# Kernel optimization log

Hardware: AMD Instinct MI355X
Metric: run time of the kernel (lower is better)

## Reference

```python
import jax, jax.numpy as jnp
import numpy as np

B, SIG, L, LAT, ENC_H, DEC_H, RHS_H, T = 256, 64, 1024, 256, 256, 512, 512, 200


def setup_inputs() -> dict:
    key = jax.random.key(0)
    ks = jax.random.split(key, 32)
    p = lambda k, s: jax.random.normal(k, s, dtype=jnp.float32) * 0.05
    inp = {
        'y': jax.random.normal(ks[0], (B, SIG, L), dtype=jnp.float32),
        't': jnp.arange(T, dtype=jnp.float32) * 0.01,
        # encoder: conv3 (OIH) + bias, res conv1 + bias, 3 layers
        'ew0': p(ks[1], (ENC_H, SIG, 3)), 'eb0': p(ks[2], (ENC_H,)),
        'rw0': p(ks[3], (ENC_H, SIG, 1)), 'rb0': p(ks[4], (ENC_H,)),
        'ew1': p(ks[5], (ENC_H, ENC_H, 3)), 'eb1': p(ks[6], (ENC_H,)),
        'rw1': p(ks[7], (ENC_H, ENC_H, 1)), 'rb1': p(ks[8], (ENC_H,)),
        'ew2': p(ks[9], (LAT, ENC_H, 3)), 'eb2': p(ks[10], (LAT,)),
        'rw2': p(ks[11], (LAT, ENC_H, 1)), 'rb2': p(ks[12], (LAT,)),
        # rhs MLP: LAT -> RHS_H -> RHS_H -> LAT
        'fw0': p(ks[13], (RHS_H, LAT)), 'fb0': p(ks[14], (RHS_H,)),
        'fw1': p(ks[15], (RHS_H, RHS_H)), 'fb1': p(ks[16], (RHS_H,)),
        'fw2': p(ks[17], (LAT, RHS_H)), 'fb2': p(ks[18], (LAT,)),
        # decoder MLP: LAT -> DEC_H -> DEC_H -> SIG
        'dw0': p(ks[19], (DEC_H, LAT)), 'db0': p(ks[20], (DEC_H,)),
        'dw1': p(ks[21], (DEC_H, DEC_H)), 'db1': p(ks[22], (DEC_H,)),
        'dw2': p(ks[23], (SIG, DEC_H)), 'db2': p(ks[24], (SIG,)),
    }
    return inp


def _conv1d(x, w, b, pad):
    out = jax.lax.conv_general_dilated(x, w, window_strides=(1,), padding=[(pad, pad)],
                                       dimension_numbers=('NCH', 'OIH', 'NCH'))
    return out + b[None, :, None]


def _forward(y, t, ew0, eb0, rw0, rb0, ew1, eb1, rw1, rb1, ew2, eb2, rw2, rb2,
             fw0, fb0, fw1, fb1, fw2, fb2, dw0, db0, dw1, db1, dw2, db2):
    # --- encoder: residual conv blocks; tanh on all but last ---
    x = y
    for (cw, cb, rw, rb, act) in [(ew0, eb0, rw0, rb0, True),
                                  (ew1, eb1, rw1, rb1, True),
                                  (ew2, eb2, rw2, rb2, False)]:
        out = _conv1d(x, cw, cb, 1)
        x = _conv1d(x, rw, rb, 0) + out
        if act:
            x = jnp.tanh(x)
    z0 = x[:, :, 0]  # [B, LAT]

    # --- RHS MLP (autonomous) ---
    def rhs(z):
        h = jnp.tanh(z @ fw0.T + fb0)
        h = jnp.tanh(h @ fw1.T + fb1)
        return h @ fw2.T + fb2

    # --- fixed-grid RK4 odeint over t ---
    def step(z, ts):
        t0, t1 = ts
        h = t1 - t0
        k1 = rhs(z)
        k2 = rhs(z + 0.5 * h * k1)
        k3 = rhs(z + 0.5 * h * k2)
        k4 = rhs(z + h * k3)
        z = z + (h / 6.0) * (k1 + 2.0 * k2 + 2.0 * k3 + k4)
        return z, z

    _, zs = jax.lax.scan(step, z0, (t[:-1], t[1:]))
    pred_z = jnp.concatenate([z0[None], zs], axis=0)  # [T, B, LAT]

    # --- decoder MLP ---
    h = jnp.tanh(pred_z @ dw0.T + db0)
    h = jnp.tanh(h @ dw1.T + db1)
    pred_y = h @ dw2.T + db2  # [T, B, SIG]
    return jnp.transpose(pred_y, (1, 2, 0))  # [B, SIG, T]


def reference(y, t, ew0, eb0, rw0, rb0, ew1, eb1, rw1, rb1, ew2, eb2, rw2, rb2,
              fw0, fb0, fw1, fb1, fw2, fb2, dw0, db0, dw1, db1, dw2, db2):
    return _forward(y, t, ew0, eb0, rw0, rb0, ew1, eb1, rw1, rb1, ew2, eb2, rw2, rb2,
                    fw0, fb0, fw1, fb1, fw2, fb2, dw0, db0, dw1, db1, dw2, db2)
```

## Files before the change

### kernel.cpp

```cpp
#include <hip/hip_runtime.h>
#include <hip/hip_bf16.h>

typedef unsigned short u16;

#define B_      256
#define SIG_    64
#define L_      1024
#define LAT_    256
#define RHSH_   512
#define T_      200

__device__ __forceinline__ bool probe_bf16(const void* tptr) {
    return ((const unsigned*)tptr)[0] != 0u;
}
__device__ __forceinline__ float ld_flex(const void* p, size_t i, bool bf) {
    return bf ? __bfloat162float(((const __hip_bfloat16*)p)[i]) : ((const float*)p)[i];
}
__device__ __forceinline__ u16 f2bf(float f) {
    unsigned x = __float_as_uint(f);
    unsigned r = x + 0x7FFFu + ((x >> 16) & 1u);
    return (u16)(r >> 16);
}
__device__ __forceinline__ float bf2f(u16 v) {
    return __uint_as_float((unsigned)v << 16);
}

static constexpr size_t Z0F  = 0;
static constexpr size_t EW0T = Z0F  + 65536;
static constexpr size_t RW0T = EW0T + 49152;
static constexpr size_t EW1T = RW0T + 16384;
static constexpr size_t RW1T = EW1T + 196608;
static constexpr size_t EW2T = RW1T + 65536;
static constexpr size_t RW2T = EW2T + 196608;
static constexpr size_t CB0  = RW2T + 65536;
static constexpr size_t CB1  = CB0 + 256;
static constexpr size_t CB2  = CB1 + 256;
static constexpr size_t TFO  = CB2 + 256;
static constexpr size_t FB0  = TFO + 256;
static constexpr size_t FB1  = FB0 + 512;
static constexpr size_t FB2  = FB1 + 512;
static constexpr size_t DB0  = FB2 + 256;
static constexpr size_t DB1  = DB0 + 512;
static constexpr size_t DB2  = DB1 + 512;
static constexpr size_t SALT = DB2 + 64;
static constexpr size_t FP32_END = SALT + 16;

static constexpr size_t FW0NS = 0;
static constexpr size_t FW1NS = FW0NS + 131072;
static constexpr size_t FW2NS = FW1NS + 262144;
static constexpr size_t DW0B  = FW2NS + 131072;
static constexpr size_t DW1B  = DW0B + 131072;
static constexpr size_t DW2B  = DW1B + 262144;
static constexpr size_t ZS    = DW2B + 32768;
static constexpr size_t US_END = ZS + 13107200;

static constexpr size_t EXCH_U64_PER_PAIR = 2048;
static constexpr size_t EXCH_OFF  = FP32_END * 4 + US_END * 2;
static constexpr size_t EXCH_BYTES = 128 * EXCH_U64_PER_PAIR * 8;
static constexpr size_t NEED_BYTES = EXCH_OFF + EXCH_BYTES;

__global__ void k_transpose(const void* __restrict__ in, float* __restrict__ out,
                            int N, int K, const void* __restrict__ tp) {
    bool bf = probe_bf16(tp);
    int idx = blockIdx.x * 256 + threadIdx.x;
    if (idx < N * K) {
        int k = idx / N;
        int n = idx - k * N;
        out[idx] = ld_flex(in, (size_t)n * K + k, bf);
    }
}

__global__ void k_prep_wns(const void* __restrict__ in, u16* __restrict__ out,
                           int N, int K, const void* __restrict__ tp) {
    bool bf = probe_bf16(tp);
    int idx = blockIdx.x * 256 + threadIdx.x;
    if (idx >= N * K) return;
    int NH = N >> 1;
    int c = idx % NH;
    int k = (idx / NH) % K;
    int h = idx / (NH * K);
    float v = ld_flex(in, (size_t)(h * NH + c) * K + k, bf);
    out[idx] = f2bf(v);
}

__global__ void k_prep_wtb(const void* __restrict__ in, u16* __restrict__ out,
                           int N, int K, const void* __restrict__ tp) {
    bool bf = probe_bf16(tp);
    int idx = blockIdx.x * 256 + threadIdx.x;
    if (idx >= N * K) return;
    int n = idx % N;
    int k = idx / N;
    out[idx] = f2bf(ld_flex(in, (size_t)n * K + k, bf));
}

__global__ void k_cvt(const void* __restrict__ in, float* __restrict__ out, int n,
                      const void* __restrict__ tp) {
    bool bf = probe_bf16(tp);
    int i = blockIdx.x * 256 + threadIdx.x;
    if (i < n) out[i] = ld_flex(in, i, bf);
}

__global__ void k_cvt_add(const void* __restrict__ a, const void* __restrict__ b,
                          float* __restrict__ out, int n, const void* __restrict__ tp) {
    bool bf = probe_bf16(tp);
    int i = blockIdx.x * 256 + threadIdx.x;
    if (i < n) out[i] = ld_flex(a, i, bf) + ld_flex(b, i, bf);
}

__global__ void k_fill(float* __restrict__ out, int n, float v) {
    int i = blockIdx.x * 256 + threadIdx.x;
    if (i < n) out[i] = v;
}

__global__ void k_bump(unsigned* p) {
    if (threadIdx.x == 0) p[0] = p[0] + 1u;
}

__global__ __launch_bounds__(256) void k_encoder(
    const void* __restrict__ y, const void* __restrict__ tp,
    const float* __restrict__ ew0T, const float* __restrict__ rw0T, const float* __restrict__ cb0,
    const float* __restrict__ ew1T, const float* __restrict__ rw1T, const float* __restrict__ cb1,
    const float* __restrict__ ew2T, const float* __restrict__ rw2T, const float* __restrict__ cb2,
    float* __restrict__ z0f) {
    bool bf = probe_bf16(tp);
    int b = blockIdx.x;
    int o = threadIdx.x;
    __shared__ float ys[64][4];
    __shared__ float x1[3][256];
    __shared__ float x2[2][256];

    {
        int i = o >> 2, l = o & 3;
        ys[i][l] = ld_flex(y, (size_t)b * SIG_ * L_ + (size_t)i * L_ + l, bf);
    }
    __syncthreads();

    {
        float a0 = 0.f, a1 = 0.f, a2 = 0.f;
        for (int i = 0; i < 64; i++) {
            float w0 = ew0T[(i * 3 + 0) * 256 + o];
            float w1 = ew0T[(i * 3 + 1) * 256 + o];
            float w2 = ew0T[(i * 3 + 2) * 256 + o];
            float rw = rw0T[i * 256 + o];
            float v0 = ys[i][0], v1 = ys[i][1], v2 = ys[i][2], v3 = ys[i][3];
            a0 += w1 * v0 + w2 * v1 + rw * v0;
            a1 += w0 * v0 + w1 * v1 + w2 * v2 + rw * v1;
            a2 += w0 * v1 + w1 * v2 + w2 * v3 + rw * v2;
        }
        float cb = cb0[o];
        x1[0][o] = tanhf(a0 + cb);
        x1[1][o] = tanhf(a1 + cb);
        x1[2][o] = tanhf(a2 + cb);
    }
    __syncthreads();

    {
        float a0 = 0.f, a1 = 0.f;
        for (int i = 0; i < 256; i++) {
            float w0 = ew1T[(i * 3 + 0) * 256 + o];
            float w1 = ew1T[(i * 3 + 1) * 256 + o];
            float w2 = ew1T[(i * 3 + 2) * 256 + o];
            float rw = rw1T[i * 256 + o];
            float v0 = x1[0][i], v1 = x1[1][i], v2 = x1[2][i];
            a0 += w1 * v0 + w2 * v1 + rw * v0;
            a1 += w0 * v0 + w1 * v1 + w2 * v2 + rw * v1;
        }
        float cb = cb1[o];
        x2[0][o] = tanhf(a0 + cb);
        x2[1][o] = tanhf(a1 + cb);
    }
    __syncthreads();

    {
        float a0 = 0.f;
        for (int i = 0; i < 256; i++) {
            float w1 = ew2T[(i * 3 + 1) * 256 + o];
            float w2 = ew2T[(i * 3 + 2) * 256 + o];
            float rw = rw2T[i * 256 + o];
            a0 += w1 * x2[0][i] + w2 * x2[1][i] + rw * x2[0][i];
        }
        z0f[(size_t)b * 256 + o] = a0 + cb2[o];
    }
}

#define RM_NONE 0
#define RM_PLAIN 1
#define RM_S1 2
#define RM_S2 3
#define RM_S34 4
#define TL_PLAIN 0
#define TL_RK 1
#define TL_K4 2

template <int KIN, int NOUT, bool ACT, int RM, int TL>
__device__ __forceinline__ void layer_ns(
    float* xs,
    const u16* __restrict__ wb,
    const float* __restrict__ bias,
    float* xo,
    float* scratch,
    unsigned long long* __restrict__ sendBuf,
    const unsigned long long* __restrict__ recvBuf,
    unsigned sendTag, unsigned recvTag, int nHalf, int tid,
    float* zbL, float* acL, float* ztL,
    float rcAC, float rcZT,
    bool tInit, float tcAC, float tcZT,
    u16* zsOut) {
    constexpr int NH  = NOUT / 2;
    constexpr int CQ  = NH / 4;
    constexpr int NPH = 512 / CQ;
    constexpr int KH  = KIN / 2;
    constexpr int KC2 = KH / NPH;
    constexpr int WK  = KH / 8;
    const int cq = tid & (CQ - 1);
    const int ph = tid / CQ;
    const int locB = nHalf * KH;
    const int remB = KH - locB;
    const u16* wl = wb + ((size_t)(locB + ph * KC2)) * NH + 4 * cq;
    const u16* wr = wb + ((size_t)(remB + ph * KC2)) * NH + 4 * cq;
    const float* xl0 = xs + locB + ph * KC2;
    const float* xl1 = xs + KIN + locB + ph * KC2;
    float4 a0 = {0.f, 0.f, 0.f, 0.f}, a1 = {0.f, 0.f, 0.f, 0.f};
#pragma unroll 4
    for (int k = 0; k < KC2; k++) {
        uint2 w = *(const uint2*)(wl + (size_t)k * NH);
        float w0 = __uint_as_float(w.x << 16);
        float w1 = __uint_as_float(w.x & 0xFFFF0000u);
        float w2 = __uint_as_float(w.y << 16);
        float w3 = __uint_as_float(w.y & 0xFFFF0000u);
        float v0 = xl0[k], v1 = xl1[k];
        a0.x += v0 * w0; a0.y += v0 * w1; a0.z += v0 * w2; a0.w += v0 * w3;
        a1.x += v1 * w0; a1.y += v1 * w1; a1.z += v1 * w2; a1.w += v1 * w3;
    }
    if constexpr (RM != RM_NONE) {
        const int lane = tid & 63;
        const int wave = tid >> 6;
        if (lane < 2 * WK) {
            const int r = lane / WK;
            const int kRel = wave * WK + (lane % WK);
            unsigned long long p;
            for (;;) {
                p = __hip_atomic_load(&recvBuf[r * KH + kRel],
                                      __ATOMIC_RELAXED, __HIP_MEMORY_SCOPE_AGENT);
                if ((unsigned)(p >> 32) == recvTag) break;
                __builtin_amdgcn_s_sleep(2);
            }
            float kv = __uint_as_float((unsigned)p);
            const int xi = r * KIN + remB + kRel;
            if constexpr (RM == RM_PLAIN) {
                xs[xi] = kv;
            } else if constexpr (RM == RM_S1) {
                xs[xi] = acL[xi] + rcAC * kv;
            } else if constexpr (RM == RM_S2) {
                float zv = zbL[xi];
                acL[xi] = zv + rcAC * kv;
                xs[xi] = zv + rcZT * kv;
            } else {
                float zv = zbL[xi];
                acL[xi] += rcAC * kv;
                xs[xi] = zv + rcZT * kv;
            }
        }
    }
    const float* xr0 = xs + remB + ph * KC2;
    const float* xr1 = xs + KIN + remB + ph * KC2;
#pragma unroll 4
    for (int k = 0; k < KC2; k++) {
        uint2 w = *(const uint2*)(wr + (size_t)k * NH);
        float w0 = __uint_as_float(w.x << 16);
        float w1 = __uint_as_float(w.x & 0xFFFF0000u);
        float w2 = __uint_as_float(w.y << 16);
        float w3 = __uint_as_float(w.y & 0xFFFF0000u);
        float v0 = xr0[k], v1 = xr1[k];
        a0.x += v0 * w0; a0.y += v0 * w1; a0.z += v0 * w2; a0.w += v0 * w3;
        a1.x += v1 * w0; a1.y += v1 * w1; a1.z += v1 * w2; a1.w += v1 * w3;
    }
    *(float4*)(scratch + (size_t)(ph * 2 + 0) * NH + 4 * cq) = a0;
    *(float4*)(scratch + (size_t)(ph * 2 + 1) * NH + 4 * cq) = a1;
    __syncthreads();
    if (tid < 2 * NH) {
        const int r = tid / NH, c = tid % NH;
        float s = 0.f;
#pragma unroll
        for (int p = 0; p < NPH; p++) s += scratch[(size_t)(p * 2 + r) * NH + c];
        s += bias[c];
        if constexpr (TL == TL_PLAIN) {
            if (ACT) s = tanhf(s);
            xo[r * NOUT + nHalf * NH + c] = s;
        }
        {
            unsigned long long packed =
                ((unsigned long long)sendTag << 32) | (unsigned long long)__float_as_uint(s);
            __hip_atomic_store(&sendBuf[r * NH + c], packed,
                               __ATOMIC_RELAXED, __HIP_MEMORY_SCOPE_AGENT);
        }
        if constexpr (TL == TL_RK) {
            const int zi = r * 256 + nHalf * NH + c;
            float zv = zbL[zi];
            acL[zi] = (tInit ? zv : acL[zi]) + tcAC * s;
            ztL[zi] = zv + tcZT * s;
        } else if constexpr (TL == TL_K4) {
            const int zi = r * 256 + nHalf * NH + c;
            float zn = acL[zi] + tcAC * s;
            zbL[zi] = zn;
            zsOut[zi] = f2bf(zn);
        }
    }
    __syncthreads();
}

__global__ __launch_bounds__(512) void k_ode_ns(
    const u16* __restrict__ fw0ns, const float* __restrict__ fb0,
    const u16* __restrict__ fw1ns, const float* __restrict__ fb1,
    const u16* __restrict__ fw2ns, const float* __restrict__ fb2,
    const float* __restrict__ tf, const float* __restrict__ z0f,
    const unsigned* __restrict__ saltp,
    u16* __restrict__ zs, unsigned long long* __restrict__ ex) {
    __shared__ __align__(16) float zb[512];
    __shared__ __align__(16) float zt[512];
    __shared__ __align__(16) float ac[512];
    __shared__ __align__(16) float h1[1024];
    __shared__ __align__(16) float h2[1024];
    __shared__ __align__(16) float scratch[4096];

    const int tid = threadIdx.x;
    const int pairId = blockIdx.x & 127;
    const int nHalf  = blockIdx.x >> 7;
    const int row0 = pairId * 2;
    unsigned long long* exBase = ex + (size_t)pairId * EXCH_U64_PER_PAIR;

    const unsigned salt = __hip_atomic_load(saltp, __ATOMIC_RELAXED, __HIP_MEMORY_SCOPE_AGENT);
    unsigned tag = salt << 13;

#define SB(t) (exBase + ((size_t)(nHalf * 2 + ((t) & 1)) * 512))
#define RB(t) ((const unsigned long long*)(exBase + ((size_t)((1 - nHalf) * 2 + ((t) & 1)) * 512)))

    const u16* fw0w = fw0ns + (size_t)nHalf * 256 * 256;
    const u16* fw1w = fw1ns + (size_t)nHalf * 512 * 256;
    const u16* fw2w = fw2ns + (size_t)nHalf * 512 * 128;
    const float* fb0o = fb0 + nHalf * 256;
    const float* fb1o = fb1 + nHalf * 256;
    const float* fb2o = fb2 + nHalf * 128;

    zb[tid] = z0f[(size_t)(row0 + (tid >> 8)) * 256 + (tid & 255)];
    __syncthreads();

    if (tid < 256) {
        int r = tid >> 7, c = tid & 127;
        zs[(size_t)(row0 + r) * 256 + nHalf * 128 + c] = f2bf(zb[r * 256 + nHalf * 128 + c]);
    }

    float h6prev = 0.f;
    unsigned tcPrev = 0;

    for (int t = 0; t < T_ - 1; t++) {
        float hstep = tf[t + 1] - tf[t];
        float hh = 0.5f * hstep;
        float h3 = hstep * (1.0f / 3.0f);
        float h6 = hstep * (1.0f / 6.0f);

        unsigned ta, tb, tc;
        ta = ++tag; tb = ++tag; tc = ++tag;
        if (t == 0)
            layer_ns<256, 512, true, RM_NONE, TL_PLAIN>(zb, fw0w, fb0o, h1, scratch,
                SB(ta), nullptr, ta, 0u, nHalf, tid, zb, ac, zt, 0.f, 0.f, false, 0.f, 0.f, nullptr);
        else
            layer_ns<256, 512, true, RM_S1, TL_PLAIN>(zb, fw0w, fb0o, h1, scratch,
                SB(ta), RB(tcPrev), ta, tcPrev, nHalf, tid, zb, ac, zt, h6prev, 0.f, false, 0.f, 0.f, nullptr);
        layer_ns<512, 512, true, RM_PLAIN, TL_PLAIN>(h1, fw1w, fb1o, h2, scratch,
            SB(tb), RB(ta), tb, ta, nHalf, tid, zb, ac, zt, 0.f, 0.f, false, 0.f, 0.f, nullptr);
        layer_ns<512, 256, false, RM_PLAIN, TL_RK>(h2, fw2w, fb2o, nullptr, scratch,
            SB(tc), RB(tb), tc, tb, nHalf, tid, zb, ac, zt, 0.f, 0.f, true, h6, hh, nullptr);
        tcPrev = tc;

        ta = ++tag; tb = ++tag; tc = ++tag;
        layer_ns<256, 512, true, RM_S2, TL_PLAIN>(zt, fw0w, fb0o, h1, scratch,
            SB(ta), RB(tcPrev), ta, tcPrev, nHalf, tid, zb, ac, zt, h6, hh, false, 0.f, 0.f, nullptr);
        layer_ns<512, 512, true, RM_PLAIN, TL_PLAIN>(h1, fw1w, fb1o, h2, scratch,
            SB(tb), RB(ta), tb, ta, nHalf, tid, zb, ac, zt, 0.f, 0.f, false, 0.f, 0.f, nullptr);
        layer_ns<512, 256, false, RM_PLAIN, TL_RK>(h2, fw2w, fb2o, nullptr, scratch,
            SB(tc), RB(tb), tc, tb, nHalf, tid, zb, ac, zt, 0.f, 0.f, false, h3, hh, nullptr);
        tcPrev = tc;

        ta = ++tag; tb = ++tag; tc = ++tag;
        layer_ns<256, 512, true, RM_S34, TL_PLAIN>(zt, fw0w, fb0o, h1, scratch,
            SB(ta), RB(tcPrev), ta, tcPrev, nHalf, tid, zb, ac, zt, h3, hh, false, 0.f, 0.f, nullptr);
        layer_ns<512, 512, true, RM_PLAIN, TL_PLAIN>(h1, fw1w, fb1o, h2, scratch,
            SB(tb), RB(ta), tb, ta, nHalf, tid, zb, ac, zt, 0.f, 0.f, false, 0.f, 0.f, nullptr);
        layer_ns<512, 256, false, RM_PLAIN, TL_RK>(h2, fw2w, fb2o, nullptr, scratch,
            SB(tc), RB(tb), tc, tb, nHalf, tid, zb, ac, zt, 0.f, 0.f, false, h3, hstep, nullptr);
        tcPrev = tc;

        ta = ++tag; tb = ++tag; tc = ++tag;
        layer_ns<256, 512, true, RM_S34, TL_PLAIN>(zt, fw0w, fb0o, h1, scratch,
            SB(ta), RB(tcPrev), ta, tcPrev, nHalf, tid, zb, ac, zt, h3, hstep, false, 0.f, 0.f, nullptr);
        layer_ns<512, 512, true, RM_PLAIN, TL_PLAIN>(h1, fw1w, fb1o, h2, scratch,
            SB(tb), RB(ta), tb, ta, nHalf, tid, zb, ac, zt, 0.f, 0.f, false, 0.f, 0.f, nullptr);
        layer_ns<512, 256, false, RM_PLAIN, TL_K4>(h2, fw2w, fb2o, nullptr, scratch,
            SB(tc), RB(tb), tc, tb, nHalf, tid, zb, ac, zt, 0.f, 0.f, false, h6, 0.f,
            zs + (size_t)(t + 1) * 65536 + (size_t)row0 * 256);
        tcPrev = tc;
        h6prev = h6;
    }
#undef SB
#undef RB
}

template <int K>
__device__ __forceinline__ void dec_layer512(
    const float* xin, const u16* __restrict__ wt, const float* __restrict__ bias,
    float* xout, int tid) {
    const int q = tid & 127;
    const int g = tid >> 7;
    const u16* wp = wt + 4 * q;
    const float* xr = xin + (size_t)g * 5 * K;
    float4 a[5];
#pragma unroll
    for (int r = 0; r < 5; r++) a[r] = {0.f, 0.f, 0.f, 0.f};
#pragma unroll 4
    for (int k = 0; k < K; k++) {
        uint2 w = *(const uint2*)(wp + (size_t)k * 512);
        float w0 = __uint_as_float(w.x << 16);
        float w1 = __uint_as_float(w.x & 0xFFFF0000u);
        float w2 = __uint_as_float(w.y << 16);
        float w3 = __uint_as_float(w.y & 0xFFFF0000u);
#pragma unroll
        for (int r = 0; r < 5; r++) {
            float v = xr[r * K + k];
            a[r].x += v * w0; a[r].y += v * w1; a[r].z += v * w2; a[r].w += v * w3;
        }
    }
    float b0 = bias[4 * q + 0], b1 = bias[4 * q + 1], b2 = bias[4 * q + 2], b3 = bias[4 * q + 3];
#pragma unroll
    for (int r = 0; r < 5; r++) {
        float4 o;
        o.x = tanhf(a[r].x + b0);
        o.y = tanhf(a[r].y + b1);
        o.z = tanhf(a[r].z + b2);
        o.w = tanhf(a[r].w + b3);
        *(float4*)(xout + (size_t)(g * 5 + r) * 512 + 4 * q) = o;
    }
}

__global__ __launch_bounds__(512) void k_decode(
    const u16* __restrict__ zs,
    const u16* __restrict__ dw0b, const float* __restrict__ db0,
    const u16* __restrict__ dw1b, const float* __restrict__ db1,
    const u16* __restrict__ dw2b, const float* __restrict__ db2,
    float* __restrict__ out) {
    __shared__ __align__(16) float xb[20 * 256];
    __shared__ __align__(16) float hh1[20 * 512];
    __shared__ __align__(16) float hh2[20 * 512];
    const int tid = threadIdx.x;
    const int b  = blockIdx.x & 255;
    const int t0 = (blockIdx.x >> 8) * 20;

    for (int i = tid; i < 20 * 256; i += 512) {
        int r = i >> 8, k = i & 255;
        xb[i] = bf2f(zs[(size_t)(t0 + r) * 65536 + (size_t)b * 256 + k]);
    }
    __syncthreads();

    dec_layer512<256>(xb, dw0b, db0, hh1, tid);
    __syncthreads();
    dec_layer512<512>(hh1, dw1b, db1, hh2, tid);
    __syncthreads();

    if (tid < 320) {
        const int q = tid & 15;
        const int r = tid >> 4;
        const u16* wp = dw2b + 4 * q;
        const float* xr = hh2 + (size_t)r * 512;
        float4 a = {0.f, 0.f, 0.f, 0.f};
#pragma unroll 4
        for (int k = 0; k < 512; k++) {
            uint2 w = *(const uint2*)(wp + (size_t)k * 64);
            float w0 = __uint_as_float(w.x << 16);
            float w1 = __uint_as_float(w.x & 0xFFFF0000u);
            float w2 = __uint_as_float(w.y << 16);
            float w3 = __uint_as_float(w.y & 0xFFFF0000u);
            float v = xr[k];
            a.x += v * w0; a.y += v * w1; a.z += v * w2; a.w += v * w3;
        }
        const int tt = t0 + r;
        out[((size_t)b * 64 + 4 * q + 0) * 200 + tt] = a.x + db2[4 * q + 0];
        out[((size_t)b * 64 + 4 * q + 1) * 200 + tt] = a.y + db2[4 * q + 1];
        out[((size_t)b * 64 + 4 * q + 2) * 200 + tt] = a.z + db2[4 * q + 2];
        out[((size_t)b * 64 + 4 * q + 3) * 200 + tt] = a.w + db2[4 * q + 3];
    }
}

#define GRID256(n) ((((n) + 255) / 256))

static const int DICT_SIZES[26] = {
    16777216, 200, 49152, 256, 16384, 256, 196608, 256, 65536, 256,
    196608, 256, 65536, 256, 131072, 512, 262144, 512, 131072, 256,
    131072, 512, 262144, 512, 32768, 64};
static const int ALPHA_SIZES[26] = {
    512, 512, 64, 131072, 262144, 32768, 256, 256, 256, 49152,
    196608, 196608, 512, 512, 256, 131072, 262144, 131072, 256, 256,
    256, 16384, 65536, 65536, 200, 16777216};
static const int ALPHA_MAP[26] = {
    25, 24, 9, 6, 21, 18, 10, 7, 22, 19, 11, 8, 23, 20, 15, 12, 16, 13, 17, 14,
    3, 0, 4, 1, 5, 2};

extern "C" void kernel_launch(void* const* d_in, const int* in_sizes, int n_in,
                              void* d_out, int out_size, void* d_ws, size_t ws_size,
                              hipStream_t stream) {
    float* out = (float*)d_out;

    bool dict_ok = (n_in == 26), alpha_ok = (n_in == 26);
    for (int i = 0; i < 26 && i < n_in; i++) {
        if (in_sizes[i] != DICT_SIZES[i]) dict_ok = false;
        if (in_sizes[i] != ALPHA_SIZES[i]) alpha_ok = false;
    }
    const void* in[26];
    if (dict_ok) {
        for (int s = 0; s < 26; s++) in[s] = d_in[s];
    } else if (alpha_ok) {
        for (int s = 0; s < 26; s++) in[s] = d_in[ALPHA_MAP[s]];
    } else {
        k_fill<<<GRID256(out_size), 256, 0, stream>>>(out, out_size, 1000.0f);
        return;
    }
    if (ws_size < NEED_BYTES) {
        k_fill<<<GRID256(out_size), 256, 0, stream>>>(out, out_size, 500.0f);
        return;
    }

    const void* y   = in[0];
    const void* t   = in[1];
    const void* ew0 = in[2];
    const void* eb0 = in[3];
    const void* rw0 = in[4];
    const void* rb0 = in[5];
    const void* ew1 = in[6];
    const void* eb1 = in[7];
    const void* rw1 = in[8];
    const void* rb1 = in[9];
    const void* ew2 = in[10];
    const void* eb2 = in[11];
    const void* rw2 = in[12];
    const void* rb2 = in[13];
    const void* fw0 = in[14];
    const void* fb0 = in[15];
    const void* fw1 = in[16];
    const void* fb1 = in[17];
    const void* fw2 = in[18];
    const void* fb2 = in[19];
    const void* dw0 = in[20];
    const void* db0 = in[21];
    const void* dw1 = in[22];
    const void* db1 = in[23];
    const void* dw2 = in[24];
    const void* db2 = in[25];

    float* ws = (float*)d_ws;
    u16* wns = (u16*)(ws + FP32_END);
    unsigned long long* ex = (unsigned long long*)((char*)d_ws + EXCH_OFF);

    k_bump<<<1, 1, 0, stream>>>((unsigned*)(ws + SALT));

    k_transpose<<<GRID256(256 * 192), 256, 0, stream>>>(ew0, ws + EW0T, 256, 192, t);
    k_transpose<<<GRID256(256 * 64),  256, 0, stream>>>(rw0, ws + RW0T, 256, 64, t);
    k_transpose<<<GRID256(256 * 768), 256, 0, stream>>>(ew1, ws + EW1T, 256, 768, t);
    k_transpose<<<GRID256(256 * 256), 256, 0, stream>>>(rw1, ws + RW1T, 256, 256, t);
    k_transpose<<<GRID256(256 * 768), 256, 0, stream>>>(ew2, ws + EW2T, 256, 768, t);
    k_transpose<<<GRID256(256 * 256), 256, 0, stream>>>(rw2, ws + RW2T, 256, 256, t);

    k_prep_wns<<<GRID256(512 * 256), 256, 0, stream>>>(fw0, wns + FW0NS, 512, 256, t);
    k_prep_wns<<<GRID256(512 * 512), 256, 0, stream>>>(fw1, wns + FW1NS, 512, 512, t);
    k_prep_wns<<<GRID256(256 * 512), 256, 0, stream>>>(fw2, wns + FW2NS, 256, 512, t);
    k_prep_wtb<<<GRID256(512 * 256), 256, 0, stream>>>(dw0, wns + DW0B, 512, 256, t);
    k_prep_wtb<<<GRID256(512 * 512), 256, 0, stream>>>(dw1, wns + DW1B, 512, 512, t);
    k_prep_wtb<<<GRID256(64 * 512),  256, 0, stream>>>(dw2, wns + DW2B, 64, 512, t);

    k_cvt<<<GRID256(512), 256, 0, stream>>>(fb0, ws + FB0, 512, t);
    k_cvt<<<GRID256(512), 256, 0, stream>>>(fb1, ws + FB1, 512, t);
    k_cvt<<<GRID256(256), 256, 0, stream>>>(fb2, ws + FB2, 256, t);
    k_cvt<<<GRID256(512), 256, 0, stream>>>(db0, ws + DB0, 512, t);
    k_cvt<<<GRID256(512), 256, 0, stream>>>(db1, ws + DB1, 512, t);
    k_cvt<<<GRID256(64),  256, 0, stream>>>(db2, ws + DB2, 64, t);
    k_cvt<<<GRID256(200), 256, 0, stream>>>(t,   ws + TFO, 200, t);
    k_cvt_add<<<GRID256(256), 256, 0, stream>>>(eb0, rb0, ws + CB0, 256, t);
    k_cvt_add<<<GRID256(256), 256, 0, stream>>>(eb1, rb1, ws + CB1, 256, t);
    k_cvt_add<<<GRID256(256), 256, 0, stream>>>(eb2, rb2, ws + CB2, 256, t);

    k_encoder<<<B_, 256, 0, stream>>>(y, t,
        ws + EW0T, ws + RW0T, ws + CB0,
        ws + EW1T, ws + RW1T, ws + CB1,
        ws + EW2T, ws + RW2T, ws + CB2,
        ws + Z0F);

    k_ode_ns<<<256, 512, 0, stream>>>(
        wns + FW0NS, ws + FB0, wns + FW1NS, ws + FB1, wns + FW2NS, ws + FB2,
        ws + TFO, ws + Z0F, (const unsigned*)(ws + SALT),
        wns + ZS, ex);

    k_decode<<<2560, 512, 0, stream>>>(
        wns + ZS, wns + DW0B, ws + DB0, wns + DW1B, ws + DB1, wns + DW2B, ws + DB2, out);
}
```

Baseline: 9.128 ms.

## Replace paired-block ODE exchange with single-row fp16 dot2 kernel and LDS weight cache

Removes the cross-block exchange, in which two blocks each computed half the outputs for two rows and synchronised through global-memory atomics with spin-waits. Now one block per batch row runs all RK4 stages alone. Weights are packed as fp16 k-pairs so the kernel can use the fdot2 instruction, activations are packed to fp16 in LDS, and part of fw1 is cached in LDS. tanhf is replaced by an exp-based fast tanh in the ODE and decoder. This removes the inter-block synchronisation latency, but each block now streams the full weight matrices, and fp16 weights and activations plus the approximate tanh reduce precision.

```diff
diff --git a/kernel.cpp b/kernel.cpp
--- a/kernel.cpp
+++ b/kernel.cpp
@@ -23,6 +23,32 @@
 }
 __device__ __forceinline__ float bf2f(u16 v) {
     return __uint_as_float((unsigned)v << 16);
+}
+
+typedef _Float16 half2_t __attribute__((ext_vector_type(2)));
+
+#if defined(__has_builtin)
+#if __has_builtin(__builtin_amdgcn_fdot2)
+#define HAVE_FDOT2 1
+#endif
+#endif
+
+__device__ __forceinline__ float fdot2(unsigned w, unsigned x, float c) {
+#ifdef HAVE_FDOT2
+    return __builtin_amdgcn_fdot2(__builtin_bit_cast(half2_t, w),
+                                  __builtin_bit_cast(half2_t, x), c, false);
+#else
+    half2_t a = __builtin_bit_cast(half2_t, w);
+    half2_t b = __builtin_bit_cast(half2_t, x);
+    return c + (float)a.x * (float)b.x + (float)a.y * (float)b.y;
+#endif
+}
+__device__ __forceinline__ unsigned pk16(float a, float b) {
+    return __builtin_bit_cast(unsigned, __builtin_amdgcn_cvt_pkrtz(a, b));
+}
+__device__ __forceinline__ float fast_tanh(float x) {
+    float e = __expf(2.0f * x);
+    return 1.0f - 2.0f / (e + 1.0f);
 }
 
 static constexpr size_t Z0F  = 0;
@@ -42,22 +68,18 @@
 static constexpr size_t DB0  = FB2 + 256;
 static constexpr size_t DB1  = DB0 + 512;
 static constexpr size_t DB2  = DB1 + 512;
-static constexpr size_t SALT = DB2 + 64;
-static constexpr size_t FP32_END = SALT + 16;
-
-static constexpr size_t FW0NS = 0;
-static constexpr size_t FW1NS = FW0NS + 131072;
-static constexpr size_t FW2NS = FW1NS + 262144;
-static constexpr size_t DW0B  = FW2NS + 131072;
+static constexpr size_t FP32_END = DB2 + 64 + 16;
+
+static constexpr size_t FW0KP = 0;
+static constexpr size_t FW1KP = FW0KP + 131072;
+static constexpr size_t FW2KP = FW1KP + 262144;
+static constexpr size_t DW0B  = FW2KP + 131072;
 static constexpr size_t DW1B  = DW0B + 131072;
 static constexpr size_t DW2B  = DW1B + 262144;
 static constexpr size_t ZS    = DW2B + 32768;
 static constexpr size_t US_END = ZS + 13107200;
 
-static constexpr size_t EXCH_U64_PER_PAIR = 2048;
-static constexpr size_t EXCH_OFF  = FP32_END * 4 + US_END * 2;
-static constexpr size_t EXCH_BYTES = 128 * EXCH_U64_PER_PAIR * 8;
-static constexpr size_t NEED_BYTES = EXCH_OFF + EXCH_BYTES;
+static constexpr size_t NEED_BYTES = FP32_END * 4 + US_END * 2;
 
 __global__ void k_transpose(const void* __restrict__ in, float* __restrict__ out,
                             int N, int K, const void* __restrict__ tp) {
@@ -70,17 +92,18 @@
     }
 }
 
-__global__ void k_prep_wns(const void* __restrict__ in, u16* __restrict__ out,
+__global__ void k_prep_wkp(const void* __restrict__ in, u16* __restrict__ out,
                            int N, int K, const void* __restrict__ tp) {
     bool bf = probe_bf16(tp);
     int idx = blockIdx.x * 256 + threadIdx.x;
     if (idx >= N * K) return;
-    int NH = N >> 1;
-    int c = idx % NH;
-    int k = (idx / NH) % K;
-    int h = idx / (NH * K);
-    float v = ld_flex(in, (size_t)(h * NH + c) * K + k, bf);
-    out[idx] = f2bf(v);
+    int kp = idx & 1;
+    int n  = (idx >> 1) % N;
+    int k2 = (idx >> 1) / N;
+    int k  = 2 * k2 + kp;
+    float v = ld_flex(in, (size_t)n * K + k, bf);
+    _Float16 hv = (_Float16)v;
+    out[idx] = *(u16*)&hv;
 }
 
 __global__ void k_prep_wtb(const void* __restrict__ in, u16* __restrict__ out,
@@ -110,10 +133,6 @@
 __global__ void k_fill(float* __restrict__ out, int n, float v) {
     int i = blockIdx.x * 256 + threadIdx.x;
     if (i < n) out[i] = v;
-}
-
-__global__ void k_bump(unsigned* p) {
-    if (threadIdx.x == 0) p[0] = p[0] + 1u;
 }
 
 __global__ __launch_bounds__(256) void k_encoder(
@@ -183,227 +202,157 @@
     }
 }
 
-#define RM_NONE 0
-#define RM_PLAIN 1
-#define RM_S1 2
-#define RM_S2 3
-#define RM_S34 4
 #define TL_PLAIN 0
 #define TL_RK 1
 #define TL_K4 2
 
-template <int KIN, int NOUT, bool ACT, int RM, int TL>
-__device__ __forceinline__ void layer_ns(
-    float* xs,
-    const u16* __restrict__ wb,
+#define DOT4(W4, XA) \
+    a.x = fdot2((W4).x, (XA), a.x); a.y = fdot2((W4).y, (XA), a.y); \
+    a.z = fdot2((W4).z, (XA), a.z); a.w = fdot2((W4).w, (XA), a.w);
+
+template <int KIN, int NOUT, bool ACT, bool ZIN, int TL, bool WC>
+__device__ __forceinline__ void layer_f(
+    const float* zin,
+    const unsigned* xpin,
+    const unsigned* __restrict__ w,
     const float* __restrict__ bias,
-    float* xo,
+    unsigned* xpo,
     float* scratch,
-    unsigned long long* __restrict__ sendBuf,
-    const unsigned long long* __restrict__ recvBuf,
-    unsigned sendTag, unsigned recvTag, int nHalf, int tid,
+    const unsigned* w1c,
+    int tid,
     float* zbL, float* acL, float* ztL,
-    float rcAC, float rcZT,
-    bool tInit, float tcAC, float tcZT,
-    u16* zsOut) {
-    constexpr int NH  = NOUT / 2;
-    constexpr int CQ  = NH / 4;
+    bool tInit, float tcAC, float tcZT, u16* zsOut) {
+    constexpr int CQ  = NOUT / 4;
     constexpr int NPH = 512 / CQ;
-    constexpr int KH  = KIN / 2;
-    constexpr int KC2 = KH / NPH;
-    constexpr int WK  = KH / 8;
+    constexpr int KC  = KIN / NPH;
+    constexpr int K2C = KC / 2;
     const int cq = tid & (CQ - 1);
     const int ph = tid / CQ;
-    const int locB = nHalf * KH;
-    const int remB = KH - locB;
-    const u16* wl = wb + ((size_t)(locB + ph * KC2)) * NH + 4 * cq;
-    const u16* wr = wb + ((size_t)(remB + ph * KC2)) * NH + 4 * cq;
-    const float* xl0 = xs + locB + ph * KC2;
-    const float* xl1 = xs + KIN + locB + ph * KC2;
-    float4 a0 = {0.f, 0.f, 0.f, 0.f}, a1 = {0.f, 0.f, 0.f, 0.f};
-#pragma unroll 4
-    for (int k = 0; k < KC2; k++) {
-        uint2 w = *(const uint2*)(wl + (size_t)k * NH);
-        float w0 = __uint_as_float(w.x << 16);
-        float w1 = __uint_as_float(w.x & 0xFFFF0000u);
-        float w2 = __uint_as_float(w.y << 16);
-        float w3 = __uint_as_float(w.y & 0xFFFF0000u);
-        float v0 = xl0[k], v1 = xl1[k];
-        a0.x += v0 * w0; a0.y += v0 * w1; a0.z += v0 * w2; a0.w += v0 * w3;
-        a1.x += v1 * w0; a1.y += v1 * w1; a1.z += v1 * w2; a1.w += v1 * w3;
-    }
-    if constexpr (RM != RM_NONE) {
-        const int lane = tid & 63;
-        const int wave = tid >> 6;
-        if (lane < 2 * WK) {
-            const int r = lane / WK;
-            const int kRel = wave * WK + (lane % WK);
-            unsigned long long p;
-            for (;;) {
-                p = __hip_atomic_load(&recvBuf[r * KH + kRel],
-                                      __ATOMIC_RELAXED, __HIP_MEMORY_SCOPE_AGENT);
-                if ((unsigned)(p >> 32) == recvTag) break;
-                __builtin_amdgcn_s_sleep(2);
+    const unsigned* wp = w + (size_t)(ph * K2C) * NOUT + 4 * cq;
+    float4 a = {0.f, 0.f, 0.f, 0.f};
+    if constexpr (ZIN) {
+        const float* x0 = zin + ph * KC;
+#pragma unroll 16
+        for (int j = 0; j < K2C; j++) {
+            uint4 w4 = *(const uint4*)(wp + (size_t)j * NOUT);
+            float2 p0 = *(const float2*)(x0 + 2 * j);
+            unsigned xa = pk16(p0.x, p0.y);
+            DOT4(w4, xa)
+        }
+    } else if constexpr (WC) {
+        const unsigned* q0 = xpin + ph * K2C;
+        if (ph == 0) {
+            const unsigned* wl = w1c + 4 * cq;
+#pragma unroll 16
+            for (int j = 0; j < K2C; j++) {
+                uint4 w4 = *(const uint4*)(wl + (size_t)j * NOUT);
+                unsigned xa = q0[j];
+                DOT4(w4, xa)
             }
-            float kv = __uint_as_float((unsigned)p);
-            const int xi = r * KIN + remB + kRel;
-            if constexpr (RM == RM_PLAIN) {
-                xs[xi] = kv;
-            } else if constexpr (RM == RM_S1) {
-                xs[xi] = acL[xi] + rcAC * kv;
-            } else if constexpr (RM == RM_S2) {
-                float zv = zbL[xi];
-                acL[xi] = zv + rcAC * kv;
-                xs[xi] = zv + rcZT * kv;
-            } else {
-                float zv = zbL[xi];
-                acL[xi] += rcAC * kv;
-                xs[xi] = zv + rcZT * kv;
+        } else {
+#pragma unroll 16
+            for (int j = 0; j < K2C; j++) {
+                uint4 w4 = *(const uint4*)(wp + (size_t)j * NOUT);
+                unsigned xa = q0[j];
+                DOT4(w4, xa)
             }
         }
-    }
-    const float* xr0 = xs + remB + ph * KC2;
-    const float* xr1 = xs + KIN + remB + ph * KC2;
-#pragma unroll 4
-    for (int k = 0; k < KC2; k++) {
-        uint2 w = *(const uint2*)(wr + (size_t)k * NH);
-        float w0 = __uint_as_float(w.x << 16);
-        float w1 = __uint_as_float(w.x & 0xFFFF0000u);
-        float w2 = __uint_as_float(w.y << 16);
-        float w3 = __uint_as_float(w.y & 0xFFFF0000u);
-        float v0 = xr0[k], v1 = xr1[k];
-        a0.x += v0 * w0; a0.y += v0 * w1; a0.z += v0 * w2; a0.w += v0 * w3;
-        a1.x += v1 * w0; a1.y += v1 * w1; a1.z += v1 * w2; a1.w += v1 * w3;
-    }
-    *(float4*)(scratch + (size_t)(ph * 2 + 0) * NH + 4 * cq) = a0;
-    *(float4*)(scratch + (size_t)(ph * 2 + 1) * NH + 4 * cq) = a1;
-    __syncthreads();
-    if (tid < 2 * NH) {
-        const int r = tid / NH, c = tid % NH;
+    } else {
+        const unsigned* q0 = xpin + ph * K2C;
+#pragma unroll 16
+        for (int j = 0; j < K2C; j++) {
+            uint4 w4 = *(const uint4*)(wp + (size_t)j * NOUT);
+            unsigned xa = q0[j];
+            DOT4(w4, xa)
+        }
+    }
+    *(float4*)(scratch + (size_t)ph * NOUT + 4 * cq) = a;
+    __syncthreads();
+    if (tid < NOUT) {
+        const int c = tid;
         float s = 0.f;
 #pragma unroll
-        for (int p = 0; p < NPH; p++) s += scratch[(size_t)(p * 2 + r) * NH + c];
+        for (int p = 0; p < NPH; p++) s += scratch[(size_t)p * NOUT + c];
         s += bias[c];
+        if (ACT) s = fast_tanh(s);
         if constexpr (TL == TL_PLAIN) {
-            if (ACT) s = tanhf(s);
-            xo[r * NOUT + nHalf * NH + c] = s;
-        }
-        {
-            unsigned long long packed =
-                ((unsigned long long)sendTag << 32) | (unsigned long long)__float_as_uint(s);
-            __hip_atomic_store(&sendBuf[r * NH + c], packed,
-                               __ATOMIC_RELAXED, __HIP_MEMORY_SCOPE_AGENT);
-        }
-        if constexpr (TL == TL_RK) {
-            const int zi = r * 256 + nHalf * NH + c;
-            float zv = zbL[zi];
-            acL[zi] = (tInit ? zv : acL[zi]) + tcAC * s;
-            ztL[zi] = zv + tcZT * s;
-        } else if constexpr (TL == TL_K4) {
-            const int zi = r * 256 + nHalf * NH + c;
-            float zn = acL[zi] + tcAC * s;
-            zbL[zi] = zn;
-            zsOut[zi] = f2bf(zn);
-        }
-    }
-    __syncthreads();
-}
-
-__global__ __launch_bounds__(512) void k_ode_ns(
-    const u16* __restrict__ fw0ns, const float* __restrict__ fb0,
-    const u16* __restrict__ fw1ns, const float* __restrict__ fb1,
-    const u16* __restrict__ fw2ns, const float* __restrict__ fb2,
+            float sn = __shfl_down(s, 1);
+            if ((tid & 1) == 0) xpo[c >> 1] = pk16(s, sn);
+        } else if constexpr (TL == TL_RK) {
+            float zv = zbL[c];
+            acL[c] = (tInit ? zv : acL[c]) + tcAC * s;
+            ztL[c] = zv + tcZT * s;
+        } else {
+            float zn = acL[c] + tcAC * s;
+            zbL[c] = zn;
+            zsOut[c] = f2bf(zn);
+        }
+    }
+    __syncthreads();
+}
+
+__global__ __launch_bounds__(512) void k_ode_f(
+    const u16* __restrict__ fw0, const float* __restrict__ fb0,
+    const u16* __restrict__ fw1, const float* __restrict__ fb1,
+    const u16* __restrict__ fw2, const float* __restrict__ fb2,
     const float* __restrict__ tf, const float* __restrict__ z0f,
-    const unsigned* __restrict__ saltp,
-    u16* __restrict__ zs, unsigned long long* __restrict__ ex) {
-    __shared__ __align__(16) float zb[512];
-    __shared__ __align__(16) float zt[512];
-    __shared__ __align__(16) float ac[512];
-    __shared__ __align__(16) float h1[1024];
-    __shared__ __align__(16) float h2[1024];
-    __shared__ __align__(16) float scratch[4096];
+    u16* __restrict__ zs) {
+    __shared__ __align__(16) float zb[256];
+    __shared__ __align__(16) float zt[256];
+    __shared__ __align__(16) float ac[256];
+    __shared__ __align__(16) unsigned h1p[256];
+    __shared__ __align__(16) unsigned h2p[256];
+    __shared__ __align__(16) float scratch[2048];
+    __shared__ __align__(16) unsigned w1c[32768];
 
     const int tid = threadIdx.x;
-    const int pairId = blockIdx.x & 127;
-    const int nHalf  = blockIdx.x >> 7;
-    const int row0 = pairId * 2;
-    unsigned long long* exBase = ex + (size_t)pairId * EXCH_U64_PER_PAIR;
-
-    const unsigned salt = __hip_atomic_load(saltp, __ATOMIC_RELAXED, __HIP_MEMORY_SCOPE_AGENT);
-    unsigned tag = salt << 13;
-
-#define SB(t) (exBase + ((size_t)(nHalf * 2 + ((t) & 1)) * 512))
-#define RB(t) ((const unsigned long long*)(exBase + ((size_t)((1 - nHalf) * 2 + ((t) & 1)) * 512)))
-
-    const u16* fw0w = fw0ns + (size_t)nHalf * 256 * 256;
-    const u16* fw1w = fw1ns + (size_t)nHalf * 512 * 256;
-    const u16* fw2w = fw2ns + (size_t)nHalf * 512 * 128;
-    const float* fb0o = fb0 + nHalf * 256;
-    const float* fb1o = fb1 + nHalf * 256;
-    const float* fb2o = fb2 + nHalf * 128;
-
-    zb[tid] = z0f[(size_t)(row0 + (tid >> 8)) * 256 + (tid & 255)];
-    __syncthreads();
-
-    if (tid < 256) {
-        int r = tid >> 7, c = tid & 127;
-        zs[(size_t)(row0 + r) * 256 + nHalf * 128 + c] = f2bf(zb[r * 256 + nHalf * 128 + c]);
-    }
-
-    float h6prev = 0.f;
-    unsigned tcPrev = 0;
+    const int row = blockIdx.x;
+    const unsigned* fw0u = (const unsigned*)fw0;
+    const unsigned* fw1u = (const unsigned*)fw1;
+    const unsigned* fw2u = (const unsigned*)fw2;
+
+    for (int i = tid * 4; i < 32768; i += 2048)
+        *(uint4*)&w1c[i] = *(const uint4*)&fw1u[i];
+
+    if (tid < 256) zb[tid] = z0f[(size_t)row * 256 + tid];
+    __syncthreads();
+    if (tid < 256) zs[(size_t)row * 256 + tid] = f2bf(zb[tid]);
 
     for (int t = 0; t < T_ - 1; t++) {
         float hstep = tf[t + 1] - tf[t];
         float hh = 0.5f * hstep;
         float h3 = hstep * (1.0f / 3.0f);
         float h6 = hstep * (1.0f / 6.0f);
-
-        unsigned ta, tb, tc;
-        ta = ++tag; tb = ++tag; tc = ++tag;
-        if (t == 0)
-            layer_ns<256, 512, true, RM_NONE, TL_PLAIN>(zb, fw0w, fb0o, h1, scratch,
-                SB(ta), nullptr, ta, 0u, nHalf, tid, zb, ac, zt, 0.f, 0.f, false, 0.f, 0.f, nullptr);
-        else
-            layer_ns<256, 512, true, RM_S1, TL_PLAIN>(zb, fw0w, fb0o, h1, scratch,
-                SB(ta), RB(tcPrev), ta, tcPrev, nHalf, tid, zb, ac, zt, h6prev, 0.f, false, 0.f, 0.f, nullptr);
-        layer_ns<512, 512, true, RM_PLAIN, TL_PLAIN>(h1, fw1w, fb1o, h2, scratch,
-            SB(tb), RB(ta), tb, ta, nHalf, tid, zb, ac, zt, 0.f, 0.f, false, 0.f, 0.f, nullptr);
-        layer_ns<512, 256, false, RM_PLAIN, TL_RK>(h2, fw2w, fb2o, nullptr, scratch,
-            SB(tc), RB(tb), tc, tb, nHalf, tid, zb, ac, zt, 0.f, 0.f, true, h6, hh, nullptr);
-        tcPrev = tc;
-
-        ta = ++tag; tb = ++tag; tc = ++tag;
-        layer_ns<256, 512, true, RM_S2, TL_PLAIN>(zt, fw0w, fb0o, h1, scratch,
-            SB(ta), RB(tcPrev), ta, tcPrev, nHalf, tid, zb, ac, zt, h6, hh, false, 0.f, 0.f, nullptr);
-        layer_ns<512, 512, true, RM_PLAIN, TL_PLAIN>(h1, fw1w, fb1o, h2, scratch,
-            SB(tb), RB(ta), tb, ta, nHalf, tid, zb, ac, zt, 0.f, 0.f, false, 0.f, 0.f, nullptr);
-        layer_ns<512, 256, false, RM_PLAIN, TL_RK>(h2, fw2w, fb2o, nullptr, scratch,
-            SB(tc), RB(tb), tc, tb, nHalf, tid, zb, ac, zt, 0.f, 0.f, false, h3, hh, nullptr);
-        tcPrev = tc;
-
-        ta = ++tag; tb = ++tag; tc = ++tag;
-        layer_ns<256, 512, true, RM_S34, TL_PLAIN>(zt, fw0w, fb0o, h1, scratch,
-            SB(ta), RB(tcPrev), ta, tcPrev, nHalf, tid, zb, ac, zt, h3, hh, false, 0.f, 0.f, nullptr);
-        layer_ns<512, 512, true, RM_PLAIN, TL_PLAIN>(h1, fw1w, fb1o, h2, scratch,
-            SB(tb), RB(ta), tb, ta, nHalf, tid, zb, ac, zt, 0.f, 0.f, false, 0.f, 0.f, nullptr);
-        layer_ns<512, 256, false, RM_PLAIN, TL_RK>(h2, fw2w, fb2o, nullptr, scratch,
-            SB(tc), RB(tb), tc, tb, nHalf, tid, zb, ac, zt, 0.f, 0.f, false, h3, hstep, nullptr);
-        tcPrev = tc;
-
-        ta = ++tag; tb = ++tag; tc = ++tag;
-        layer_ns<256, 512, true, RM_S34, TL_PLAIN>(zt, fw0w, fb0o, h1, scratch,
-            SB(ta), RB(tcPrev), ta, tcPrev, nHalf, tid, zb, ac, zt, h3, hstep, false, 0.f, 0.f, nullptr);
-        layer_ns<512, 512, true, RM_PLAIN, TL_PLAIN>(h1, fw1w, fb1o, h2, scratch,
-            SB(tb), RB(ta), tb, ta, nHalf, tid, zb, ac, zt, 0.f, 0.f, false, 0.f, 0.f, nullptr);
-        layer_ns<512, 256, false, RM_PLAIN, TL_K4>(h2, fw2w, fb2o, nullptr, scratch,
-            SB(tc), RB(tb), tc, tb, nHalf, tid, zb, ac, zt, 0.f, 0.f, false, h6, 0.f,
-            zs + (size_t)(t + 1) * 65536 + (size_t)row0 * 256);
-        tcPrev = tc;
-        h6prev = h6;
-    }
-#undef SB
-#undef RB
+        u16* zo = zs + (size_t)(t + 1) * 65536 + (size_t)row * 256;
+
+        layer_f<256, 512, true , true , TL_PLAIN, false>(zb, nullptr, fw0u, fb0, h1p,
+            scratch, nullptr, tid, zb, ac, zt, false, 0.f, 0.f, nullptr);
+        layer_f<512, 512, true , false, TL_PLAIN, true >(nullptr, h1p, fw1u, fb1, h2p,
+            scratch, w1c, tid, zb, ac, zt, false, 0.f, 0.f, nullptr);
+        layer_f<512, 256, false, false, TL_RK  , false>(nullptr, h2p, fw2u, fb2, nullptr,
+            scratch, nullptr, tid, zb, ac, zt, true, h6, hh, nullptr);
+
+        layer_f<256, 512, true , true , TL_PLAIN, false>(zt, nullptr, fw0u, fb0, h1p,
+            scratch, nullptr, tid, zb, ac, zt, false, 0.f, 0.f, nullptr);
+        layer_f<512, 512, true , false, TL_PLAIN, true >(nullptr, h1p, fw1u, fb1, h2p,
+            scratch, w1c, tid, zb, ac, zt, false, 0.f, 0.f, nullptr);
+        layer_f<512, 256, false, false, TL_RK  , false>(nullptr, h2p, fw2u, fb2, nullptr,
+            scratch, nullptr, tid, zb, ac, zt, false, h3, hh, nullptr);
+
+        layer_f<256, 512, true , true , TL_PLAIN, false>(zt, nullptr, fw0u, fb0, h1p,
+            scratch, nullptr, tid, zb, ac, zt, false, 0.f, 0.f, nullptr);
+        layer_f<512, 512, true , false, TL_PLAIN, true >(nullptr, h1p, fw1u, fb1, h2p,
+            scratch, w1c, tid, zb, ac, zt, false, 0.f, 0.f, nullptr);
+        layer_f<512, 256, false, false, TL_RK  , false>(nullptr, h2p, fw2u, fb2, nullptr,
+            scratch, nullptr, tid, zb, ac, zt, false, h3, hstep, nullptr);
+
+        layer_f<256, 512, true , true , TL_PLAIN, false>(zt, nullptr, fw0u, fb0, h1p,
+            scratch, nullptr, tid, zb, ac, zt, false, 0.f, 0.f, nullptr);
+        layer_f<512, 512, true , false, TL_PLAIN, true >(nullptr, h1p, fw1u, fb1, h2p,
+            scratch, w1c, tid, zb, ac, zt, false, 0.f, 0.f, nullptr);
+        layer_f<512, 256, false, false, TL_K4  , false>(nullptr, h2p, fw2u, fb2, nullptr,
+            scratch, nullptr, tid, zb, ac, zt, false, h6, 0.f, zo);
+    }
 }
 
 template <int K>
@@ -434,10 +383,10 @@
 #pragma unroll
     for (int r = 0; r < 5; r++) {
         float4 o;
-        o.x = tanhf(a[r].x + b0);
-        o.y = tanhf(a[r].y + b1);
-        o.z = tanhf(a[r].z + b2);
-        o.w = tanhf(a[r].w + b3);
+        o.x = fast_tanh(a[r].x + b0);
+        o.y = fast_tanh(a[r].y + b1);
+        o.z = fast_tanh(a[r].z + b2);
+        o.w = fast_tanh(a[r].w + b3);
         *(float4*)(xout + (size_t)(g * 5 + r) * 512 + 4 * q) = o;
     }
 }
@@ -557,9 +506,6 @@
 
     float* ws = (float*)d_ws;
     u16* wns = (u16*)(ws + FP32_END);
-    unsigned long long* ex = (unsigned long long*)((char*)d_ws + EXCH_OFF);
-
-    k_bump<<<1, 1, 0, stream>>>((unsigned*)(ws + SALT));
 
     k_transpose<<<GRID256(256 * 192), 256, 0, stream>>>(ew0, ws + EW0T, 256, 192, t);
     k_transpose<<<GRID256(256 * 64),  256, 0, stream>>>(rw0, ws + RW0T, 256, 64, t);
@@ -568,9 +514,9 @@
     k_transpose<<<GRID256(256 * 768), 256, 0, stream>>>(ew2, ws + EW2T, 256, 768, t);
     k_transpose<<<GRID256(256 * 256), 256, 0, stream>>>(rw2, ws + RW2T, 256, 256, t);
 
-    k_prep_wns<<<GRID256(512 * 256), 256, 0, stream>>>(fw0, wns + FW0NS, 512, 256, t);
-    k_prep_wns<<<GRID256(512 * 512), 256, 0, stream>>>(fw1, wns + FW1NS, 512, 512, t);
-    k_prep_wns<<<GRID256(256 * 512), 256, 0, stream>>>(fw2, wns + FW2NS, 256, 512, t);
+    k_prep_wkp<<<GRID256(512 * 256), 256, 0, stream>>>(fw0, wns + FW0KP, 512, 256, t);
+    k_prep_wkp<<<GRID256(512 * 512), 256, 0, stream>>>(fw1, wns + FW1KP, 512, 512, t);
+    k_prep_wkp<<<GRID256(256 * 512), 256, 0, stream>>>(fw2, wns + FW2KP, 256, 512, t);
     k_prep_wtb<<<GRID256(512 * 256), 256, 0, stream>>>(dw0, wns + DW0B, 512, 256, t);
     k_prep_wtb<<<GRID256(512 * 512), 256, 0, stream>>>(dw1, wns + DW1B, 512, 512, t);
     k_prep_wtb<<<GRID256(64 * 512),  256, 0, stream>>>(dw2, wns + DW2B, 64, 512, t);
@@ -592,10 +538,9 @@
         ws + EW2T, ws + RW2T, ws + CB2,
         ws + Z0F);
 
-    k_ode_ns<<<256, 512, 0, stream>>>(
-        wns + FW0NS, ws + FB0, wns + FW1NS, ws + FB1, wns + FW2NS, ws + FB2,
-        ws + TFO, ws + Z0F, (const unsigned*)(ws + SALT),
-        wns + ZS, ex);
+    k_ode_f<<<B_, 512, 0, stream>>>(
+        wns + FW0KP, ws + FB0, wns + FW1KP, ws + FB1, wns + FW2KP, ws + FB2,
+        ws + TFO, ws + Z0F, wns + ZS);
 
     k_decode<<<2560, 512, 0, stream>>>(
         wns + ZS, wns + DW0B, ws + DB0, wns + DW1B, ws + DB1, wns + DW2B, ws + DB2, out);
```

New measurement: 7.506 ms, median of 2. 1.22x faster.
